# Kernel optimization log

Hardware: AMD Instinct MI355X
Metric: run time of the kernel (lower is better)

The kernel has to match this reference:

```python
import jax, jax.numpy as jnp
import numpy as np

N_NODES = 50000
N_EDGES = 600000
N_GRAPHS = 64
IN_C, HID_C, OUT_C = 128, 128, 64


def gcn_conv(x, edge_index, W, b, num_nodes):
    """PyG GCNConv: x' = D^-1/2 (A + I) D^-1/2 (x W) + b, messages src->dst."""
    src, dst = edge_index[0], edge_index[1]
    # add self-loops
    loop = jnp.arange(num_nodes, dtype=src.dtype)
    src_full = jnp.concatenate([src, loop])
    dst_full = jnp.concatenate([dst, loop])
    # degree of A+I counted at the aggregation (dst) side
    deg = jax.ops.segment_sum(jnp.ones_like(dst_full, dtype=x.dtype), dst_full,
                              num_segments=num_nodes)
    dinv = jax.lax.rsqrt(jnp.maximum(deg, 1.0))
    norm = dinv[src_full] * dinv[dst_full]              # [E+N]
    h = x @ W                                           # [N, C_out] dense GEMM
    msg = h[src_full] * norm[:, None]                   # gather + scale
    out = jax.ops.segment_sum(msg, dst_full, num_segments=num_nodes)  # scatter-add
    return out + b


def global_mean_pool(x, batch, num_graphs):
    s = jax.ops.segment_sum(x, batch, num_segments=num_graphs)
    cnt = jax.ops.segment_sum(jnp.ones_like(batch, dtype=x.dtype), batch,
                              num_segments=num_graphs)
    return s / jnp.maximum(cnt, 1.0)[:, None]


def setup_inputs() -> dict:
    key = jax.random.key(0)
    ks = jax.random.split(key, 8)
    x = jax.random.normal(ks[0], (N_NODES, IN_C), dtype=jnp.float32)
    edge_index = jax.random.randint(ks[1], (2, N_EDGES), 0, N_NODES, dtype=jnp.int64)
    batch = jnp.sort(jax.random.randint(ks[2], (N_NODES,), 0, N_GRAPHS, dtype=jnp.int64))
    # Glorot-style init like PyG defaults
    W1 = jax.random.normal(ks[3], (IN_C, HID_C), dtype=jnp.float32) * (1.0 / np.sqrt(IN_C))
    b1 = jnp.zeros((HID_C,), dtype=jnp.float32)
    W2 = jax.random.normal(ks[4], (HID_C, OUT_C), dtype=jnp.float32) * (1.0 / np.sqrt(HID_C))
    b2 = jnp.zeros((OUT_C,), dtype=jnp.float32)
    return {"x": x, "W1": W1, "b1": b1, "W2": W2, "b2": b2,
            "edge_index": edge_index, "batch": batch}


def reference(x, W1, b1, W2, b2, edge_index, batch):
    h = gcn_conv(x, edge_index, W1, b1, N_NODES)
    h = jax.nn.relu(h)
    h = gcn_conv(h, edge_index, W2, b2, N_NODES)
    return global_mean_pool(h, batch, N_GRAPHS)  # [N_GRAPHS, OUT_C]
```

## Files before the change

### kernel.cpp

```cpp
#include <hip/hip_runtime.h>

#define NN 50000
#define NE 600000
#define NG 64
#define SCAN_T 1024
#define SCAN_NB ((NN + SCAN_T - 1) / SCAN_T)

typedef unsigned int uint_t;
typedef unsigned short ushort_t;
typedef __attribute__((ext_vector_type(8))) short bf16x8;
typedef __attribute__((ext_vector_type(4))) float f32x4;

__device__ __forceinline__ ushort_t f2bf(float x) {
    uint_t u = __builtin_bit_cast(uint_t, x);
    u = (u + 0x7FFFu + ((u >> 16) & 1u)) >> 16;
    return (ushort_t)u;
}
__device__ __forceinline__ float bf_lo(uint_t p) {
    uint_t v = p << 16; return __builtin_bit_cast(float, v);
}
__device__ __forceinline__ float bf_hi(uint_t p) {
    uint_t v = p & 0xFFFF0000u; return __builtin_bit_cast(float, v);
}

__global__ void k_prep(const float* __restrict__ W1, const float* __restrict__ W2,
                       int* __restrict__ deg, float* __restrict__ psum,
                       ushort_t* __restrict__ W1t, ushort_t* __restrict__ W2t) {
    int i = blockIdx.x * blockDim.x + threadIdx.x;
    if (i < NN) deg[i] = 0;
    if (i < NG * 64) psum[i] = 0.f;
    if (i < 128 * 128) {
        int k = i >> 7, n = i & 127;
        W1t[n * 128 + k] = f2bf(W1[i]);
    }
    if (i < 128 * 64) {
        int k = i >> 6, n = i & 63;
        W2t[n * 128 + k] = f2bf(W2[i]);
    }
}

__global__ void k_hist(const int* __restrict__ dst, int* __restrict__ deg) {
    int e = blockIdx.x * blockDim.x + threadIdx.x;
    if (e < NE) atomicAdd(&deg[dst[e]], 1);
}

__global__ __launch_bounds__(SCAN_T) void k_scan1(const int* __restrict__ deg,
                                                  int* __restrict__ blockSums) {
    __shared__ int s[SCAN_T];
    int i = blockIdx.x * SCAN_T + threadIdx.x;
    s[threadIdx.x] = (i < NN) ? deg[i] : 0;
    __syncthreads();
    for (int off = SCAN_T / 2; off > 0; off >>= 1) {
        if (threadIdx.x < off) s[threadIdx.x] += s[threadIdx.x + off];
        __syncthreads();
    }
    if (threadIdx.x == 0) blockSums[blockIdx.x] = s[0];
}

__global__ __launch_bounds__(SCAN_T) void k_scan3(const int* __restrict__ deg,
                                                  const int* __restrict__ blockSums,
                                                  int* __restrict__ rowptr,
                                                  int* __restrict__ cursor,
                                                  float* __restrict__ dinv) {
    __shared__ int offs[64];
    __shared__ int s[SCAN_T];
    const int t = threadIdx.x;
    if (t < 64) {
        int orig = (t < SCAN_NB) ? blockSums[t] : 0;
        int v = orig;
        for (int off = 1; off < 64; off <<= 1) {
            int u = __shfl_up(v, off);
            if (t >= off) v += u;
        }
        offs[t] = v - orig;
    }
    const int i = blockIdx.x * SCAN_T + t;
    const int v = (i < NN) ? deg[i] : 0;
    s[t] = v;
    __syncthreads();
    for (int off = 1; off < SCAN_T; off <<= 1) {
        int u = (t >= off) ? s[t - off] : 0;
        int cur = s[t];
        __syncthreads();
        s[t] = cur + u;
        __syncthreads();
    }
    if (i < NN) {
        int ex = offs[blockIdx.x] + s[t] - v;
        rowptr[i] = ex;
        cursor[i] = ex;
        dinv[i] = rsqrtf((float)(v + 1));
    }
    if (i == 0) rowptr[NN] = NE;
}

__global__ void k_scatter(const int* __restrict__ src, const int* __restrict__ dst,
                          int* __restrict__ cursor, int* __restrict__ csr_src) {
    int e = blockIdx.x * blockDim.x + threadIdx.x;
    if (e >= NE) return;
    int d = dst[e];
    int p = atomicAdd(&cursor[d], 1);
    csr_src[p] = src[e];
}

__global__ __launch_bounds__(256) void k_gemm_mfma(const float* __restrict__ X,
                                                   const ushort_t* __restrict__ Wt,
                                                   const float* __restrict__ dinv,
                                                   ushort_t* __restrict__ Hb) {
    __shared__ ushort_t xs[128 * 128];
    __shared__ ushort_t ws[128 * 128];
    const int tid = threadIdx.x;
    const int row0 = blockIdx.x * 128;

    for (int idx = tid; idx < 128 * 32; idx += 256) {
        int r = idx >> 5, c4 = idx & 31;
        int row = row0 + r;
        float4 v = make_float4(0.f, 0.f, 0.f, 0.f);
        if (row < NN) v = ((const float4*)X)[(long)row * 32 + c4];
        ushort4 o;
        o.x = f2bf(v.x); o.y = f2bf(v.y); o.z = f2bf(v.z); o.w = f2bf(v.w);
        uint_t byte = (uint_t)(r * 256 + c4 * 8) ^ (uint_t)((r & 7) << 4);
        *(ushort4*)((char*)xs + byte) = o;
    }
    for (int idx = tid; idx < 128 * 16; idx += 256) {
        int n = idx >> 4, c16 = idx & 15;
        uint4 v = ((const uint4*)Wt)[idx];
        uint_t byte = (uint_t)(n * 256 + c16 * 16) ^ (uint_t)((n & 7) << 4);
        *(uint4*)((char*)ws + byte) = v;
    }
    __syncthreads();

    const int w = tid >> 6;
    const int l = tid & 63;
    const int m0 = (w >> 1) * 4;
    const int n0 = (w & 1) * 4;
    const int lr = l & 15;
    const int kg = l >> 4;

    f32x4 acc[4][4] = {};
    for (int kk = 0; kk < 4; ++kk) {
        const int kb = kk * 64 + kg * 16;
        bf16x8 a[4], b[4];
#pragma unroll
        for (int m = 0; m < 4; ++m) {
            int r = (m0 + m) * 16 + lr;
            uint_t byte = (uint_t)(r * 256 + kb) ^ (uint_t)((r & 7) << 4);
            a[m] = *(const bf16x8*)((const char*)xs + byte);
        }
#pragma unroll
        for (int n = 0; n < 4; ++n) {
            int r = (n0 + n) * 16 + lr;
            uint_t byte = (uint_t)(r * 256 + kb) ^ (uint_t)((r & 7) << 4);
            b[n] = *(const bf16x8*)((const char*)ws + byte);
        }
#pragma unroll
        for (int m = 0; m < 4; ++m)
#pragma unroll
            for (int n = 0; n < 4; ++n)
                acc[m][n] = __builtin_amdgcn_mfma_f32_16x16x32_bf16(a[m], b[n], acc[m][n], 0, 0, 0);
    }

#pragma unroll
    for (int m = 0; m < 4; ++m) {
#pragma unroll
        for (int r = 0; r < 4; ++r) {
            int row = row0 + (m0 + m) * 16 + kg * 4 + r;
            if (row < NN) {
                float sc = dinv[row];
#pragma unroll
                for (int n = 0; n < 4; ++n) {
                    int col = (n0 + n) * 16 + lr;
                    Hb[(long)row * 128 + col] = f2bf(acc[m][n][r] * sc);
                }
            }
        }
    }
}

__global__ __launch_bounds__(256) void k_gemm_mfma2(const ushort_t* __restrict__ H1,
                                                    const ushort_t* __restrict__ W2t,
                                                    const float* __restrict__ dinv,
                                                    ushort_t* __restrict__ G) {
    __shared__ ushort_t xs[128 * 128];
    __shared__ ushort_t ws2[64 * 128];
    const int tid = threadIdx.x;
    const int row0 = blockIdx.x * 128;

    for (int idx = tid; idx < 128 * 16; idx += 256) {
        int r = idx >> 4, c16 = idx & 15;
        int row = row0 + r;
        uint4 v = make_uint4(0u, 0u, 0u, 0u);
        if (row < NN) v = ((const uint4*)H1)[(long)row * 16 + c16];
        uint_t byte = (uint_t)(r * 256 + c16 * 16) ^ (uint_t)((r & 7) << 4);
        *(uint4*)((char*)xs + byte) = v;
    }
    for (int idx = tid; idx < 64 * 16; idx += 256) {
        int n = idx >> 4, c16 = idx & 15;
        uint4 v = ((const uint4*)W2t)[idx];
        uint_t byte = (uint_t)(n * 256 + c16 * 16) ^ (uint_t)((n & 7) << 4);
        *(uint4*)((char*)ws2 + byte) = v;
    }
    __syncthreads();

    const int w = tid >> 6;
    const int l = tid & 63;
    const int lr = l & 15;
    const int kg = l >> 4;
    const int m0 = w * 2;

    f32x4 acc[2][4] = {};
    for (int kk = 0; kk < 4; ++kk) {
        const int kb = kk * 64 + kg * 16;
        bf16x8 a[2], b[4];
#pragma unroll
        for (int m = 0; m < 2; ++m) {
            int r = (m0 + m) * 16 + lr;
            uint_t byte = (uint_t)(r * 256 + kb) ^ (uint_t)((r & 7) << 4);
            a[m] = *(const bf16x8*)((const char*)xs + byte);
        }
#pragma unroll
        for (int n = 0; n < 4; ++n) {
            int r = n * 16 + lr;
            uint_t byte = (uint_t)(r * 256 + kb) ^ (uint_t)((r & 7) << 4);
            b[n] = *(const bf16x8*)((const char*)ws2 + byte);
        }
#pragma unroll
        for (int m = 0; m < 2; ++m)
#pragma unroll
            for (int n = 0; n < 4; ++n)
                acc[m][n] = __builtin_amdgcn_mfma_f32_16x16x32_bf16(a[m], b[n], acc[m][n], 0, 0, 0);
    }

#pragma unroll
    for (int m = 0; m < 2; ++m) {
#pragma unroll
        for (int r = 0; r < 4; ++r) {
            int row = row0 + (m0 + m) * 16 + kg * 4 + r;
            if (row < NN) {
                float sc = dinv[row];
#pragma unroll
                for (int n = 0; n < 4; ++n) {
                    int col = n * 16 + lr;
                    G[(long)row * 64 + col] = f2bf(acc[m][n][r] * sc);
                }
            }
        }
    }
}

__global__ __launch_bounds__(256) void k_agg1(const int* __restrict__ rowptr,
                                              const int* __restrict__ csr_src,
                                              const float* __restrict__ dinv,
                                              const ushort_t* __restrict__ Hb,
                                              const float* __restrict__ bias,
                                              ushort_t* __restrict__ OUT) {
    constexpr int TPN = 16;
    constexpr int NPB = 256 / TPN;
    const int node = blockIdx.x * NPB + threadIdx.x / TPN;
    if (node >= NN) return;
    const int lane = threadIdx.x % TPN;
    const float dd = dinv[node];
    const uint4* __restrict__ H4 = (const uint4*)Hb;

    float a0, a1, a2, a3, a4, a5, a6, a7;
    {
        uint4 sv = H4[(long)node * TPN + lane];
        a0 = bf_lo(sv.x); a1 = bf_hi(sv.x);
        a2 = bf_lo(sv.y); a3 = bf_hi(sv.y);
        a4 = bf_lo(sv.z); a5 = bf_hi(sv.z);
        a6 = bf_lo(sv.w); a7 = bf_hi(sv.w);
    }

    const int beg = rowptr[node], end = rowptr[node + 1];
    int k = beg;
    const int n4 = beg + ((end - beg) & ~3);
    for (; k < n4; k += 4) {
        int s0 = csr_src[k + 0];
        int s1 = csr_src[k + 1];
        int s2 = csr_src[k + 2];
        int s3 = csr_src[k + 3];
        uint4 h0 = H4[(long)s0 * TPN + lane];
        uint4 h1 = H4[(long)s1 * TPN + lane];
        uint4 h2 = H4[(long)s2 * TPN + lane];
        uint4 h3 = H4[(long)s3 * TPN + lane];
        a0 += (bf_lo(h0.x) + bf_lo(h1.x)) + (bf_lo(h2.x) + bf_lo(h3.x));
        a1 += (bf_hi(h0.x) + bf_hi(h1.x)) + (bf_hi(h2.x) + bf_hi(h3.x));
        a2 += (bf_lo(h0.y) + bf_lo(h1.y)) + (bf_lo(h2.y) + bf_lo(h3.y));
        a3 += (bf_hi(h0.y) + bf_hi(h1.y)) + (bf_hi(h2.y) + bf_hi(h3.y));
        a4 += (bf_lo(h0.z) + bf_lo(h1.z)) + (bf_lo(h2.z) + bf_lo(h3.z));
        a5 += (bf_hi(h0.z) + bf_hi(h1.z)) + (bf_hi(h2.z) + bf_hi(h3.z));
        a6 += (bf_lo(h0.w) + bf_lo(h1.w)) + (bf_lo(h2.w) + bf_lo(h3.w));
        a7 += (bf_hi(h0.w) + bf_hi(h1.w)) + (bf_hi(h2.w) + bf_hi(h3.w));
    }
    for (; k < end; ++k) {
        int s = csr_src[k];
        uint4 h = H4[(long)s * TPN + lane];
        a0 += bf_lo(h.x); a1 += bf_hi(h.x);
        a2 += bf_lo(h.y); a3 += bf_hi(h.y);
        a4 += bf_lo(h.z); a5 += bf_hi(h.z);
        a6 += bf_lo(h.w); a7 += bf_hi(h.w);
    }

    a0 *= dd; a1 *= dd; a2 *= dd; a3 *= dd;
    a4 *= dd; a5 *= dd; a6 *= dd; a7 *= dd;

    const float4 b0 = *(const float4*)&bias[lane * 8];
    const float4 b1 = *(const float4*)&bias[lane * 8 + 4];
    a0 = fmaxf(a0 + b0.x, 0.f); a1 = fmaxf(a1 + b0.y, 0.f);
    a2 = fmaxf(a2 + b0.z, 0.f); a3 = fmaxf(a3 + b0.w, 0.f);
    a4 = fmaxf(a4 + b1.x, 0.f); a5 = fmaxf(a5 + b1.y, 0.f);
    a6 = fmaxf(a6 + b1.z, 0.f); a7 = fmaxf(a7 + b1.w, 0.f);

    uint4 o;
    o.x = (uint_t)f2bf(a0) | ((uint_t)f2bf(a1) << 16);
    o.y = (uint_t)f2bf(a2) | ((uint_t)f2bf(a3) << 16);
    o.z = (uint_t)f2bf(a4) | ((uint_t)f2bf(a5) << 16);
    o.w = (uint_t)f2bf(a6) | ((uint_t)f2bf(a7) << 16);
    ((uint4*)OUT)[(long)node * TPN + lane] = o;
}

__global__ __launch_bounds__(256) void k_agg2pool(const int* __restrict__ rowptr,
                                                  const int* __restrict__ csr_src,
                                                  const float* __restrict__ dinv,
                                                  const ushort_t* __restrict__ Gb,
                                                  const int* __restrict__ batch,
                                                  float* __restrict__ psum) {
    constexpr int TPN = 8;
    constexpr int NPB = 32;
    const int nodeLocal = threadIdx.x / TPN;
    const int node = blockIdx.x * NPB + nodeLocal;
    const int lane = threadIdx.x % TPN;
    __shared__ float vsh[NPB][64 + 1];
    __shared__ int gsh[NPB];

    if (node < NN) {
        const float dd = dinv[node];
        const uint4* __restrict__ H4 = (const uint4*)Gb;

        float a0, a1, a2, a3, a4, a5, a6, a7;
        {
            uint4 sv = H4[(long)node * TPN + lane];
            a0 = bf_lo(sv.x); a1 = bf_hi(sv.x);
            a2 = bf_lo(sv.y); a3 = bf_hi(sv.y);
            a4 = bf_lo(sv.z); a5 = bf_hi(sv.z);
            a6 = bf_lo(sv.w); a7 = bf_hi(sv.w);
        }
        const int beg = rowptr[node], end = rowptr[node + 1];
        int k = beg;
        const int n4 = beg + ((end - beg) & ~3);
        for (; k < n4; k += 4) {
            int s0 = csr_src[k + 0];
            int s1 = csr_src[k + 1];
            int s2 = csr_src[k + 2];
            int s3 = csr_src[k + 3];
            uint4 h0 = H4[(long)s0 * TPN + lane];
            uint4 h1 = H4[(long)s1 * TPN + lane];
            uint4 h2 = H4[(long)s2 * TPN + lane];
            uint4 h3 = H4[(long)s3 * TPN + lane];
            a0 += (bf_lo(h0.x) + bf_lo(h1.x)) + (bf_lo(h2.x) + bf_lo(h3.x));
            a1 += (bf_hi(h0.x) + bf_hi(h1.x)) + (bf_hi(h2.x) + bf_hi(h3.x));
            a2 += (bf_lo(h0.y) + bf_lo(h1.y)) + (bf_lo(h2.y) + bf_lo(h3.y));
            a3 += (bf_hi(h0.y) + bf_hi(h1.y)) + (bf_hi(h2.y) + bf_hi(h3.y));
            a4 += (bf_lo(h0.z) + bf_lo(h1.z)) + (bf_lo(h2.z) + bf_lo(h3.z));
            a5 += (bf_hi(h0.z) + bf_hi(h1.z)) + (bf_hi(h2.z) + bf_hi(h3.z));
            a6 += (bf_lo(h0.w) + bf_lo(h1.w)) + (bf_lo(h2.w) + bf_lo(h3.w));
            a7 += (bf_hi(h0.w) + bf_hi(h1.w)) + (bf_hi(h2.w) + bf_hi(h3.w));
        }
        for (; k < end; ++k) {
            int s = csr_src[k];
            uint4 h = H4[(long)s * TPN + lane];
            a0 += bf_lo(h.x); a1 += bf_hi(h.x);
            a2 += bf_lo(h.y); a3 += bf_hi(h.y);
            a4 += bf_lo(h.z); a5 += bf_hi(h.z);
            a6 += bf_lo(h.w); a7 += bf_hi(h.w);
        }
        float* vp = &vsh[nodeLocal][lane * 8];
        vp[0] = a0 * dd; vp[1] = a1 * dd; vp[2] = a2 * dd; vp[3] = a3 * dd;
        vp[4] = a4 * dd; vp[5] = a5 * dd; vp[6] = a6 * dd; vp[7] = a7 * dd;
        if (lane == 0) gsh[nodeLocal] = batch[node];
    } else {
        if (lane == 0) gsh[nodeLocal] = -1;
    }
    __syncthreads();

    if (threadIdx.x < 64) {
        const int ch = threadIdx.x;
        float acc = 0.f;
        int gprev = -1;
        for (int n = 0; n < NPB; ++n) {
            int g = gsh[n];
            if (g != gprev) {
                if (gprev >= 0) unsafeAtomicAdd(&psum[gprev * 64 + ch], acc);
                acc = 0.f;
                gprev = g;
            }
            if (g >= 0) acc += vsh[n][ch];
        }
        if (gprev >= 0) unsafeAtomicAdd(&psum[gprev * 64 + ch], acc);
    }
}

__global__ __launch_bounds__(64) void k_pool2(const float* __restrict__ psum,
                                              const int* __restrict__ batch,
                                              const float* __restrict__ b2,
                                              float* __restrict__ out) {
    const int g = blockIdx.x;
    const int ch = threadIdx.x;
    int beg, end;
    {
        int lo = 0, hi = NN;
        while (lo < hi) { int mid = (lo + hi) >> 1; if (batch[mid] < g) lo = mid + 1; else hi = mid; }
        beg = lo;
        lo = beg; hi = NN;
        while (lo < hi) { int mid = (lo + hi) >> 1; if (batch[mid] < g + 1) lo = mid + 1; else hi = mid; }
        end = lo;
    }
    int cnt = end - beg;
    out[g * 64 + ch] = (cnt > 0) ? (psum[g * 64 + ch] / (float)cnt + b2[ch]) : 0.f;
}

extern "C" void kernel_launch(void* const* d_in, const int* in_sizes, int n_in,
                              void* d_out, int out_size, void* d_ws, size_t ws_size,
                              hipStream_t stream) {
    const float* x  = (const float*)d_in[0];
    const float* W1 = (const float*)d_in[1];
    const float* b1 = (const float*)d_in[2];
    const float* W2 = (const float*)d_in[3];
    const float* b2 = (const float*)d_in[4];
    const int* ei   = (const int*)d_in[5];
    const int* src  = (const int*)ei;
    const int* dst  = (const int*)(ei + NE);
    const int* batch = (const int*)d_in[6];
    float* out = (float*)d_out;

    char* p = (char*)d_ws;
    int* deg       = (int*)p;          p += (size_t)NN * 4;
    int* rowptr    = (int*)p;          p += (size_t)(NN + 4) * 4;
    int* cursor    = (int*)p;          p += (size_t)NN * 4;
    int* csr_src   = (int*)p;          p += (size_t)NE * 4;
    int* blockSums = (int*)p;          p += (size_t)64 * 4;
    float* dinv    = (float*)p;        p += (size_t)NN * 4;
    float* psum    = (float*)p;        p += (size_t)NG * 64 * 4;
    ushort_t* W1t  = (ushort_t*)p;     p += (size_t)128 * 128 * 2;
    ushort_t* W2t  = (ushort_t*)p;     p += (size_t)64 * 128 * 2;
    ushort_t* Hb   = (ushort_t*)p;     p += (size_t)NN * 128 * 2;
    ushort_t* H1b  = (ushort_t*)p;     p += (size_t)NN * 128 * 2;
    ushort_t* Gb   = (ushort_t*)p;     p += (size_t)NN * 64 * 2;

    k_prep<<<(NN + 255) / 256, 256, 0, stream>>>(W1, W2, deg, psum, W1t, W2t);
    k_hist<<<(NE + 255) / 256, 256, 0, stream>>>(dst, deg);
    k_scan1<<<SCAN_NB, SCAN_T, 0, stream>>>(deg, blockSums);
    k_scan3<<<SCAN_NB, SCAN_T, 0, stream>>>(deg, blockSums, rowptr, cursor, dinv);
    k_scatter<<<(NE + 255) / 256, 256, 0, stream>>>(src, dst, cursor, csr_src);

    k_gemm_mfma<<<(NN + 127) / 128, 256, 0, stream>>>(x, W1t, dinv, Hb);
    k_agg1<<<(NN + 15) / 16, 256, 0, stream>>>(rowptr, csr_src, dinv, Hb, b1, H1b);

    k_gemm_mfma2<<<(NN + 127) / 128, 256, 0, stream>>>(H1b, W2t, dinv, Gb);
    k_agg2pool<<<(NN + 31) / 32, 256, 0, stream>>>(rowptr, csr_src, dinv, Gb, batch, psum);

    k_pool2<<<NG, 64, 0, stream>>>(psum, batch, b2, out);
}
```

Baseline: 155.2 us.

## Fuse layer-1 aggregation with layer-2 GEMM via shared-memory tile

Merges the first-layer neighbour aggregation (bias, ReLU, bf16 pack) with the second-layer MFMA GEMM into one kernel. Aggregated rows go into a swizzled LDS tile of 32 nodes, and the block then multiplies that tile by W2 directly. This removes the H1 intermediate buffer's global write and re-read and one kernel launch. In exchange, each node now uses 8 threads instead of 16, and every block reloads W2 into LDS for only 32 rows, so the GEMM part is less efficient.

```diff
diff --git a/kernel.cpp b/kernel.cpp
--- a/kernel.cpp
+++ b/kernel.cpp
@@ -177,146 +177,132 @@
     }
 }
 
-__global__ __launch_bounds__(256) void k_gemm_mfma2(const ushort_t* __restrict__ H1,
-                                                    const ushort_t* __restrict__ W2t,
-                                                    const float* __restrict__ dinv,
-                                                    ushort_t* __restrict__ G) {
-    __shared__ ushort_t xs[128 * 128];
+__global__ __launch_bounds__(256) void k_agg1g2(const int* __restrict__ rowptr,
+                                                const int* __restrict__ csr_src,
+                                                const float* __restrict__ dinv,
+                                                const ushort_t* __restrict__ Hb,
+                                                const float* __restrict__ bias,
+                                                const ushort_t* __restrict__ W2t,
+                                                ushort_t* __restrict__ G) {
+    constexpr int TPN = 8;
+    constexpr int NPB = 32;
+    __shared__ ushort_t hsh[NPB * 128];
     __shared__ ushort_t ws2[64 * 128];
     const int tid = threadIdx.x;
-    const int row0 = blockIdx.x * 128;
-
-    for (int idx = tid; idx < 128 * 16; idx += 256) {
-        int r = idx >> 4, c16 = idx & 15;
-        int row = row0 + r;
-        uint4 v = make_uint4(0u, 0u, 0u, 0u);
-        if (row < NN) v = ((const uint4*)H1)[(long)row * 16 + c16];
-        uint_t byte = (uint_t)(r * 256 + c16 * 16) ^ (uint_t)((r & 7) << 4);
-        *(uint4*)((char*)xs + byte) = v;
-    }
+    const int row0 = blockIdx.x * NPB;
+    const int nodeLocal = tid / TPN;
+    const int node = row0 + nodeLocal;
+    const int lane = tid % TPN;
+
     for (int idx = tid; idx < 64 * 16; idx += 256) {
         int n = idx >> 4, c16 = idx & 15;
         uint4 v = ((const uint4*)W2t)[idx];
         uint_t byte = (uint_t)(n * 256 + c16 * 16) ^ (uint_t)((n & 7) << 4);
         *(uint4*)((char*)ws2 + byte) = v;
     }
+
+    float a[16];
+    if (node < NN) {
+        const float dd = dinv[node];
+        const uint2* __restrict__ H2 = (const uint2*)Hb;
+        const long base = (long)node * 32;
+#pragma unroll
+        for (int q = 0; q < 4; ++q) {
+            uint2 h = H2[base + lane * 4 + q];
+            a[q * 4 + 0] = bf_lo(h.x); a[q * 4 + 1] = bf_hi(h.x);
+            a[q * 4 + 2] = bf_lo(h.y); a[q * 4 + 3] = bf_hi(h.y);
+        }
+        const int beg = rowptr[node], end = rowptr[node + 1];
+        int k = beg;
+        const int n2 = beg + ((end - beg) & ~1);
+        for (; k < n2; k += 2) {
+            long b0 = (long)csr_src[k] * 16 + lane * 2;
+            long b1 = (long)csr_src[k + 1] * 16 + lane * 2;
+            uint4 h0 = ((const uint4*)Hb)[b0];
+            uint4 h1 = ((const uint4*)Hb)[b0 + 1];
+            uint4 h2 = ((const uint4*)Hb)[b1];
+            uint4 h3 = ((const uint4*)Hb)[b1 + 1];
+            a[0] += bf_lo(h0.x) + bf_lo(h2.x); a[1] += bf_hi(h0.x) + bf_hi(h2.x);
+            a[2] += bf_lo(h0.y) + bf_lo(h2.y); a[3] += bf_hi(h0.y) + bf_hi(h2.y);
+            a[4] += bf_lo(h0.z) + bf_lo(h2.z); a[5] += bf_hi(h0.z) + bf_hi(h2.z);
+            a[6] += bf_lo(h0.w) + bf_lo(h2.w); a[7] += bf_hi(h0.w) + bf_hi(h2.w);
+            a[8]  += bf_lo(h1.x) + bf_lo(h3.x); a[9]  += bf_hi(h1.x) + bf_hi(h3.x);
+            a[10] += bf_lo(h1.y) + bf_lo(h3.y); a[11] += bf_hi(h1.y) + bf_hi(h3.y);
+            a[12] += bf_lo(h1.z) + bf_lo(h3.z); a[13] += bf_hi(h1.z) + bf_hi(h3.z);
+            a[14] += bf_lo(h1.w) + bf_lo(h3.w); a[15] += bf_hi(h1.w) + bf_hi(h3.w);
+        }
+        for (; k < end; ++k) {
+            long b0 = (long)csr_src[k] * 16 + lane * 2;
+            uint4 h0 = ((const uint4*)Hb)[b0];
+            uint4 h1 = ((const uint4*)Hb)[b0 + 1];
+            a[0] += bf_lo(h0.x); a[1] += bf_hi(h0.x);
+            a[2] += bf_lo(h0.y); a[3] += bf_hi(h0.y);
+            a[4] += bf_lo(h0.z); a[5] += bf_hi(h0.z);
+            a[6] += bf_lo(h0.w); a[7] += bf_hi(h0.w);
+            a[8]  += bf_lo(h1.x); a[9]  += bf_hi(h1.x);
+            a[10] += bf_lo(h1.y); a[11] += bf_hi(h1.y);
+            a[12] += bf_lo(h1.z); a[13] += bf_hi(h1.z);
+            a[14] += bf_lo(h1.w); a[15] += bf_hi(h1.w);
+        }
+#pragma unroll
+        for (int q = 0; q < 4; ++q) {
+            float4 bb = *(const float4*)&bias[lane * 16 + q * 4];
+            float v0 = fmaxf(a[q * 4 + 0] * dd + bb.x, 0.f);
+            float v1 = fmaxf(a[q * 4 + 1] * dd + bb.y, 0.f);
+            float v2 = fmaxf(a[q * 4 + 2] * dd + bb.z, 0.f);
+            float v3 = fmaxf(a[q * 4 + 3] * dd + bb.w, 0.f);
+            ushort4 o;
+            o.x = f2bf(v0); o.y = f2bf(v1); o.z = f2bf(v2); o.w = f2bf(v3);
+            uint_t byte = (uint_t)(nodeLocal * 256 + lane * 32 + q * 8)
+                        ^ (uint_t)((nodeLocal & 7) << 4);
+            *(ushort4*)((char*)hsh + byte) = o;
+        }
+    } else {
+#pragma unroll
+        for (int q = 0; q < 4; ++q) {
+            ushort4 o = {0, 0, 0, 0};
+            uint_t byte = (uint_t)(nodeLocal * 256 + lane * 32 + q * 8)
+                        ^ (uint_t)((nodeLocal & 7) << 4);
+            *(ushort4*)((char*)hsh + byte) = o;
+        }
+    }
     __syncthreads();
 
     const int w = tid >> 6;
     const int l = tid & 63;
     const int lr = l & 15;
     const int kg = l >> 4;
-    const int m0 = w * 2;
-
-    f32x4 acc[2][4] = {};
+    const int mt = w >> 1;
+    const int nt0 = (w & 1) * 2;
+
+    f32x4 acc[2] = {};
     for (int kk = 0; kk < 4; ++kk) {
         const int kb = kk * 64 + kg * 16;
-        bf16x8 a[2], b[4];
-#pragma unroll
-        for (int m = 0; m < 2; ++m) {
-            int r = (m0 + m) * 16 + lr;
-            uint_t byte = (uint_t)(r * 256 + kb) ^ (uint_t)((r & 7) << 4);
-            a[m] = *(const bf16x8*)((const char*)xs + byte);
-        }
-#pragma unroll
-        for (int n = 0; n < 4; ++n) {
-            int r = n * 16 + lr;
-            uint_t byte = (uint_t)(r * 256 + kb) ^ (uint_t)((r & 7) << 4);
-            b[n] = *(const bf16x8*)((const char*)ws2 + byte);
-        }
-#pragma unroll
-        for (int m = 0; m < 2; ++m)
-#pragma unroll
-            for (int n = 0; n < 4; ++n)
-                acc[m][n] = __builtin_amdgcn_mfma_f32_16x16x32_bf16(a[m], b[n], acc[m][n], 0, 0, 0);
-    }
-
-#pragma unroll
-    for (int m = 0; m < 2; ++m) {
+        int ra = mt * 16 + lr;
+        uint_t ba = (uint_t)(ra * 256 + kb) ^ (uint_t)((ra & 7) << 4);
+        bf16x8 afrag = *(const bf16x8*)((const char*)hsh + ba);
+#pragma unroll
+        for (int j = 0; j < 2; ++j) {
+            int rb = (nt0 + j) * 16 + lr;
+            uint_t bb = (uint_t)(rb * 256 + kb) ^ (uint_t)((rb & 7) << 4);
+            bf16x8 bfrag = *(const bf16x8*)((const char*)ws2 + bb);
+            acc[j] = __builtin_amdgcn_mfma_f32_16x16x32_bf16(afrag, bfrag, acc[j], 0, 0, 0);
+        }
+    }
+
+    float sc[4];
+    int rowb = row0 + mt * 16 + kg * 4;
+#pragma unroll
+    for (int r = 0; r < 4; ++r) sc[r] = (rowb + r < NN) ? dinv[rowb + r] : 0.f;
+#pragma unroll
+    for (int j = 0; j < 2; ++j) {
+        int col = (nt0 + j) * 16 + lr;
 #pragma unroll
         for (int r = 0; r < 4; ++r) {
-            int row = row0 + (m0 + m) * 16 + kg * 4 + r;
-            if (row < NN) {
-                float sc = dinv[row];
-#pragma unroll
-                for (int n = 0; n < 4; ++n) {
-                    int col = n * 16 + lr;
-                    G[(long)row * 64 + col] = f2bf(acc[m][n][r] * sc);
-                }
-            }
-        }
-    }
-}
-
-__global__ __launch_bounds__(256) void k_agg1(const int* __restrict__ rowptr,
-                                              const int* __restrict__ csr_src,
-                                              const float* __restrict__ dinv,
-                                              const ushort_t* __restrict__ Hb,
-                                              const float* __restrict__ bias,
-                                              ushort_t* __restrict__ OUT) {
-    constexpr int TPN = 16;
-    constexpr int NPB = 256 / TPN;
-    const int node = blockIdx.x * NPB + threadIdx.x / TPN;
-    if (node >= NN) return;
-    const int lane = threadIdx.x % TPN;
-    const float dd = dinv[node];
-    const uint4* __restrict__ H4 = (const uint4*)Hb;
-
-    float a0, a1, a2, a3, a4, a5, a6, a7;
-    {
-        uint4 sv = H4[(long)node * TPN + lane];
-        a0 = bf_lo(sv.x); a1 = bf_hi(sv.x);
-        a2 = bf_lo(sv.y); a3 = bf_hi(sv.y);
-        a4 = bf_lo(sv.z); a5 = bf_hi(sv.z);
-        a6 = bf_lo(sv.w); a7 = bf_hi(sv.w);
-    }
-
-    const int beg = rowptr[node], end = rowptr[node + 1];
-    int k = beg;
-    const int n4 = beg + ((end - beg) & ~3);
-    for (; k < n4; k += 4) {
-        int s0 = csr_src[k + 0];
-        int s1 = csr_src[k + 1];
-        int s2 = csr_src[k + 2];
-        int s3 = csr_src[k + 3];
-        uint4 h0 = H4[(long)s0 * TPN + lane];
-        uint4 h1 = H4[(long)s1 * TPN + lane];
-        uint4 h2 = H4[(long)s2 * TPN + lane];
-        uint4 h3 = H4[(long)s3 * TPN + lane];
-        a0 += (bf_lo(h0.x) + bf_lo(h1.x)) + (bf_lo(h2.x) + bf_lo(h3.x));
-        a1 += (bf_hi(h0.x) + bf_hi(h1.x)) + (bf_hi(h2.x) + bf_hi(h3.x));
-        a2 += (bf_lo(h0.y) + bf_lo(h1.y)) + (bf_lo(h2.y) + bf_lo(h3.y));
-        a3 += (bf_hi(h0.y) + bf_hi(h1.y)) + (bf_hi(h2.y) + bf_hi(h3.y));
-        a4 += (bf_lo(h0.z) + bf_lo(h1.z)) + (bf_lo(h2.z) + bf_lo(h3.z));
-        a5 += (bf_hi(h0.z) + bf_hi(h1.z)) + (bf_hi(h2.z) + bf_hi(h3.z));
-        a6 += (bf_lo(h0.w) + bf_lo(h1.w)) + (bf_lo(h2.w) + bf_lo(h3.w));
-        a7 += (bf_hi(h0.w) + bf_hi(h1.w)) + (bf_hi(h2.w) + bf_hi(h3.w));
-    }
-    for (; k < end; ++k) {
-        int s = csr_src[k];
-        uint4 h = H4[(long)s * TPN + lane];
-        a0 += bf_lo(h.x); a1 += bf_hi(h.x);
-        a2 += bf_lo(h.y); a3 += bf_hi(h.y);
-        a4 += bf_lo(h.z); a5 += bf_hi(h.z);
-        a6 += bf_lo(h.w); a7 += bf_hi(h.w);
-    }
-
-    a0 *= dd; a1 *= dd; a2 *= dd; a3 *= dd;
-    a4 *= dd; a5 *= dd; a6 *= dd; a7 *= dd;
-
-    const float4 b0 = *(const float4*)&bias[lane * 8];
-    const float4 b1 = *(const float4*)&bias[lane * 8 + 4];
-    a0 = fmaxf(a0 + b0.x, 0.f); a1 = fmaxf(a1 + b0.y, 0.f);
-    a2 = fmaxf(a2 + b0.z, 0.f); a3 = fmaxf(a3 + b0.w, 0.f);
-    a4 = fmaxf(a4 + b1.x, 0.f); a5 = fmaxf(a5 + b1.y, 0.f);
-    a6 = fmaxf(a6 + b1.z, 0.f); a7 = fmaxf(a7 + b1.w, 0.f);
-
-    uint4 o;
-    o.x = (uint_t)f2bf(a0) | ((uint_t)f2bf(a1) << 16);
-    o.y = (uint_t)f2bf(a2) | ((uint_t)f2bf(a3) << 16);
-    o.z = (uint_t)f2bf(a4) | ((uint_t)f2bf(a5) << 16);
-    o.w = (uint_t)f2bf(a6) | ((uint_t)f2bf(a7) << 16);
-    ((uint4*)OUT)[(long)node * TPN + lane] = o;
+            int row = rowb + r;
+            if (row < NN) G[(long)row * 64 + col] = f2bf(acc[j][r] * sc[r]);
+        }
+    }
 }
 
 __global__ __launch_bounds__(256) void k_agg2pool(const int* __restrict__ rowptr,
@@ -444,7 +430,6 @@
     ushort_t* W1t  = (ushort_t*)p;     p += (size_t)128 * 128 * 2;
     ushort_t* W2t  = (ushort_t*)p;     p += (size_t)64 * 128 * 2;
     ushort_t* Hb   = (ushort_t*)p;     p += (size_t)NN * 128 * 2;
-    ushort_t* H1b  = (ushort_t*)p;     p += (size_t)NN * 128 * 2;
     ushort_t* Gb   = (ushort_t*)p;     p += (size_t)NN * 64 * 2;
 
     k_prep<<<(NN + 255) / 256, 256, 0, stream>>>(W1, W2, deg, psum, W1t, W2t);
@@ -454,9 +439,9 @@
     k_scatter<<<(NE + 255) / 256, 256, 0, stream>>>(src, dst, cursor, csr_src);
 
     k_gemm_mfma<<<(NN + 127) / 128, 256, 0, stream>>>(x, W1t, dinv, Hb);
-    k_agg1<<<(NN + 15) / 16, 256, 0, stream>>>(rowptr, csr_src, dinv, Hb, b1, H1b);
-
-    k_gemm_mfma2<<<(NN + 127) / 128, 256, 0, stream>>>(H1b, W2t, dinv, Gb);
+
+    k_agg1g2<<<(NN + 31) / 32, 256, 0, stream>>>(rowptr, csr_src, dinv, Hb, b1, W2t, Gb);
+
     k_agg2pool<<<(NN + 31) / 32, 256, 0, stream>>>(rowptr, csr_src, dinv, Gb, batch, psum);
 
     k_pool2<<<NG, 64, 0, stream>>>(psum, batch, b2, out);
```

Measured after the change: 153.7 us (median of 2 runs). No clear change (-1.0%).
